# Kernel optimization log

Measured on AMD Instinct MI355X. Metric: run time of the kernel, lower is better.

Reference implementation:

```python
import jax, jax.numpy as jnp
import numpy as np

N_NODES = 50000
N_EDGES = 300000
F_IN, HID, N_CLS = 256, 256, 128


def _glorot_linear(key, fan_in, fan_out):
    # torch.nn.Linear-style uniform init, kaiming bound 1/sqrt(fan_in)
    s = 1.0 / np.sqrt(fan_in)
    return jax.random.uniform(key, (fan_in, fan_out), jnp.float32, -s, s)


def setup_inputs() -> dict:
    key = jax.random.key(0)
    ks = jax.random.split(key, 8)
    x = jax.random.normal(ks[0], (N_NODES, F_IN), jnp.float32)
    edge_index = jax.random.randint(ks[1], (2, N_EDGES), 0, N_NODES, dtype=jnp.int32)
    return {
        "x": x,
        "edge_index": edge_index,
        "W1": _glorot_linear(ks[2], F_IN, HID), "b1": jnp.zeros((HID,), jnp.float32),
        "W2": _glorot_linear(ks[3], HID, HID),  "b2": jnp.zeros((HID,), jnp.float32),
        "W3": _glorot_linear(ks[4], HID, HID),  "b3": jnp.zeros((HID,), jnp.float32),
        "W4": _glorot_linear(ks[5], HID, N_CLS), "b4": jnp.zeros((N_CLS,), jnp.float32),
    }


def _gcn_conv(x, W, b, src, dst, norm, n):
    # x' = D^{-1/2} (A + I) D^{-1/2} X W + b   (PyG GCNConv default)
    h = x @ W                                  # [N, out]
    msg = h[src] * norm[:, None]               # gather + edge scaling  [E', out]
    return jax.ops.segment_sum(msg, dst, num_segments=n) + b


def reference(x, edge_index, W1, b1, W2, b2, W3, b3, W4, b4):
    n = x.shape[0]
    loops = jnp.arange(n, dtype=edge_index.dtype)
    src = jnp.concatenate([edge_index[0], loops])  # add self-loops
    dst = jnp.concatenate([edge_index[1], loops])
    # symmetric normalization: deg over target nodes (unit edge weights)
    deg = jax.ops.segment_sum(jnp.ones_like(dst, jnp.float32), dst, num_segments=n)
    dis = jnp.where(deg > 0, jax.lax.rsqrt(jnp.maximum(deg, 1.0)), 0.0)
    norm = dis[src] * dis[dst]                     # [E']

    h = jax.nn.relu(_gcn_conv(x, W1, b1, src, dst, norm, n))
    h = jax.nn.relu(_gcn_conv(h, W2, b2, src, dst, norm, n))
    h = jax.nn.relu(_gcn_conv(h, W3, b3, src, dst, norm, n))
    h = _gcn_conv(h, W4, b4, src, dst, norm, n)    # [N, C]

    # global_add_pool with batch == zeros -> single-graph sum pool
    pooled = jnp.sum(h, axis=0, keepdims=True)     # [1, C]
    return (pooled, jax.nn.log_softmax(pooled, axis=1))
```

## Files before the change

### kernel.cpp

```cpp
#include <hip/hip_runtime.h>


typedef __attribute__((ext_vector_type(8))) short short8;
typedef __attribute__((ext_vector_type(4))) short short4v;
typedef __attribute__((ext_vector_type(4))) float float4v;

__device__ __forceinline__ unsigned short f2b(float f) {
    unsigned int u = __builtin_bit_cast(unsigned int, f);
    u += 0x7fffu + ((u >> 16) & 1u);
    return (unsigned short)(u >> 16);
}
__device__ __forceinline__ float b2f(unsigned short b) {
    unsigned int u = ((unsigned int)b) << 16;
    return __builtin_bit_cast(float, u);
}


__global__ void zero_kernel(int* __restrict__ cnt, float* __restrict__ tsum,
                            float* __restrict__ acc, int N) {
    int i = blockIdx.x * 256 + threadIdx.x;
    if (i < N) { cnt[i] = 0; tsum[i] = 0.f; }
    if (i < 256) acc[i] = 0.f;
}

__global__ void count_kernel(const int* __restrict__ dst, int* __restrict__ cnt, int E) {
    int i = blockIdx.x * blockDim.x + threadIdx.x;
    if (i < E) atomicAdd(&cnt[dst[i]], 1);
}

__global__ void blocksum_kernel(const int* __restrict__ cnt, int* __restrict__ bsum, int N) {
    __shared__ int s[256];
    int t = threadIdx.x;
    int i = blockIdx.x * 256 + t;
    s[t] = (i < N) ? cnt[i] : 0;
    __syncthreads();
    for (int d = 128; d > 0; d >>= 1) {
        if (t < d) s[t] += s[t + d];
        __syncthreads();
    }
    if (t == 0) bsum[blockIdx.x] = s[0];
}

__global__ void bscan_kernel(int* __restrict__ bsum, int B) {
    __shared__ int s[256];
    int t = threadIdx.x;
    int v = (t < B) ? bsum[t] : 0;
    s[t] = v;
    __syncthreads();
    for (int d = 1; d < 256; d <<= 1) {
        int x = (t >= d) ? s[t - d] : 0;
        __syncthreads();
        s[t] += x;
        __syncthreads();
    }
    if (t < B) bsum[t] = s[t] - v;
}

__global__ void finalize_kernel(const int* __restrict__ cnt, const int* __restrict__ bsum,
                                int* __restrict__ offs, int* __restrict__ cursor,
                                float* __restrict__ dis, int N, int E) {
    __shared__ int s[256];
    int t = threadIdx.x;
    int i = blockIdx.x * 256 + t;
    int c = (i < N) ? cnt[i] : 0;
    s[t] = c;
    __syncthreads();
    for (int d = 1; d < 256; d <<= 1) {
        int x = (t >= d) ? s[t - d] : 0;
        __syncthreads();
        s[t] += x;
        __syncthreads();
    }
    if (i < N) {
        int ex = bsum[blockIdx.x] + s[t] - c;
        offs[i] = ex;
        cursor[i] = ex;
        dis[i] = rsqrtf((float)(c + 1));
    }
    if (blockIdx.x == 0 && t == 0) offs[N] = E;
}

__global__ void scatter_outsum_kernel(const int* __restrict__ src, const int* __restrict__ dst,
                                      const float* __restrict__ dis, int* __restrict__ cursor,
                                      int* __restrict__ csr_src, float* __restrict__ csr_nrm,
                                      float* __restrict__ tsum, int E) {
    int i = blockIdx.x * blockDim.x + threadIdx.x;
    if (i < E) {
        int s = src[i], d = dst[i];
        float dd = dis[d];
        int pos = atomicAdd(&cursor[d], 1);
        csr_src[pos] = s;
        csr_nrm[pos] = dis[s] * dd;
        atomicAdd(&tsum[s], dd);
    }
}


__global__ void convert_wt_kernel(const float* __restrict__ W1, const float* __restrict__ W2,
                                  const float* __restrict__ W3, unsigned short* __restrict__ Wt1,
                                  unsigned short* __restrict__ Wt2, unsigned short* __restrict__ Wt3) {
    const float* W = (blockIdx.y == 0) ? W1 : (blockIdx.y == 1) ? W2 : W3;
    unsigned short* Wt = (blockIdx.y == 0) ? Wt1 : (blockIdx.y == 1) ? Wt2 : Wt3;
    int n = blockIdx.x;
    int k = threadIdx.x;
    Wt[n * 256 + k] = f2b(W[k * 256 + n]);
}

template <int AFP32>
__global__ __launch_bounds__(256, 3) void gemm_bf16_kernel(
        const void* __restrict__ Ap, const unsigned short* __restrict__ Wt,
        unsigned short* __restrict__ C, int M) {
    __shared__ unsigned short As[128 * 72];
    __shared__ unsigned short Bs[128 * 72];
    const int tid = threadIdx.x;
    const int lane = tid & 63;
    const int wave = tid >> 6;
    const int l15 = lane & 15;
    const int quad = lane >> 4;
    const int wm = wave & 1;
    const int wn = wave >> 1;
    const int m0 = blockIdx.x * 128;
    const int n0 = blockIdx.y * 128;

    float4v acc[4][4] = {};

    const int srow = tid >> 3;
    const int skof = (tid & 7) * 8;

    for (int kk = 0; kk < 256; kk += 64) {
#pragma unroll
        for (int p = 0; p < 4; p++) {
            int row = p * 32 + srow;
            int gm = m0 + row;
            if (AFP32) {
                const float* Af = (const float*)Ap;
                float4 lo = make_float4(0.f, 0.f, 0.f, 0.f);
                float4 hi = make_float4(0.f, 0.f, 0.f, 0.f);
                if (gm < M) {
                    lo = *(const float4*)&Af[(size_t)gm * 256 + kk + skof];
                    hi = *(const float4*)&Af[(size_t)gm * 256 + kk + skof + 4];
                }
                union { unsigned short u[8]; float4 v; } pk;
                pk.u[0] = f2b(lo.x); pk.u[1] = f2b(lo.y);
                pk.u[2] = f2b(lo.z); pk.u[3] = f2b(lo.w);
                pk.u[4] = f2b(hi.x); pk.u[5] = f2b(hi.y);
                pk.u[6] = f2b(hi.z); pk.u[7] = f2b(hi.w);
                *(float4*)&As[row * 72 + skof] = pk.v;
            } else {
                const unsigned short* Ab = (const unsigned short*)Ap;
                float4 av = make_float4(0.f, 0.f, 0.f, 0.f);
                if (gm < M) av = *(const float4*)&Ab[(size_t)gm * 256 + kk + skof];
                *(float4*)&As[row * 72 + skof] = av;
            }
            float4 bv = *(const float4*)&Wt[(size_t)(n0 + row) * 256 + kk + skof];
            *(float4*)&Bs[row * 72 + skof] = bv;
        }
        __syncthreads();
#pragma unroll
        for (int ks = 0; ks < 64; ks += 32) {
            short8 af[4], bf[4];
#pragma unroll
            for (int mi = 0; mi < 4; mi++)
                af[mi] = *(const short8*)&As[(wm * 64 + mi * 16 + l15) * 72 + ks + quad * 8];
#pragma unroll
            for (int nj = 0; nj < 4; nj++)
                bf[nj] = *(const short8*)&Bs[(wn * 64 + nj * 16 + l15) * 72 + ks + quad * 8];
#pragma unroll
            for (int mi = 0; mi < 4; mi++)
#pragma unroll
                for (int nj = 0; nj < 4; nj++)
                    acc[mi][nj] = __builtin_amdgcn_mfma_f32_16x16x32_bf16(
                        af[mi], bf[nj], acc[mi][nj], 0, 0, 0);
        }
        __syncthreads();
    }

#pragma unroll
    for (int mi = 0; mi < 4; mi++) {
#pragma unroll
        for (int r = 0; r < 4; r++) {
            int row = m0 + wm * 64 + mi * 16 + quad * 4 + r;
            if (row < M) {
#pragma unroll
                for (int nj = 0; nj < 4; nj++) {
                    int col = n0 + wn * 64 + nj * 16 + l15;
                    C[(size_t)row * 256 + col] = f2b(acc[mi][nj][r]);
                }
            }
        }
    }
}

template <int RELU>
__global__ __launch_bounds__(256) void agg_bf16_kernel(
        const unsigned short* __restrict__ T, const float* __restrict__ bias,
        const int* __restrict__ offs, const int* __restrict__ csr_src,
        const float* __restrict__ csr_nrm, const float* __restrict__ dis,
        unsigned short* __restrict__ out, int N) {
    int v = blockIdx.x * 8 + (threadIdx.x >> 5);
    if (v >= N) return;
    int l = threadIdx.x & 31;
    int f8 = l * 8;
    int beg = offs[v], end = offs[v + 1];
    float dv = dis[v];
    float w = dv * dv;
    float a[8];
    {
        short8 hs = *(const short8*)&T[(size_t)v * 256 + f8];
#pragma unroll
        for (int i = 0; i < 8; i++) a[i] = w * b2f((unsigned short)hs[i]);
    }
    int e = beg;
    for (; e + 4 <= end; e += 4) {
        int s0 = csr_src[e],     s1 = csr_src[e + 1];
        int s2 = csr_src[e + 2], s3 = csr_src[e + 3];
        float n0 = csr_nrm[e],     n1 = csr_nrm[e + 1];
        float n2 = csr_nrm[e + 2], n3 = csr_nrm[e + 3];
        short8 h0 = *(const short8*)&T[(size_t)s0 * 256 + f8];
        short8 h1 = *(const short8*)&T[(size_t)s1 * 256 + f8];
        short8 h2 = *(const short8*)&T[(size_t)s2 * 256 + f8];
        short8 h3 = *(const short8*)&T[(size_t)s3 * 256 + f8];
#pragma unroll
        for (int i = 0; i < 8; i++)
            a[i] += n0 * b2f((unsigned short)h0[i]) + n1 * b2f((unsigned short)h1[i])
                  + n2 * b2f((unsigned short)h2[i]) + n3 * b2f((unsigned short)h3[i]);
    }
    for (; e < end; e++) {
        int s = csr_src[e];
        float nm = csr_nrm[e];
        short8 h = *(const short8*)&T[(size_t)s * 256 + f8];
#pragma unroll
        for (int i = 0; i < 8; i++) a[i] += nm * b2f((unsigned short)h[i]);
    }
    float4 bv0 = *(const float4*)&bias[f8];
    float4 bv1 = *(const float4*)&bias[f8 + 4];
    a[0] += bv0.x; a[1] += bv0.y; a[2] += bv0.z; a[3] += bv0.w;
    a[4] += bv1.x; a[5] += bv1.y; a[6] += bv1.z; a[7] += bv1.w;
    if (RELU) {
#pragma unroll
        for (int i = 0; i < 8; i++) a[i] = fmaxf(a[i], 0.f);
    }
    uint4 o;
    o.x = (unsigned int)f2b(a[0]) | ((unsigned int)f2b(a[1]) << 16);
    o.y = (unsigned int)f2b(a[2]) | ((unsigned int)f2b(a[3]) << 16);
    o.z = (unsigned int)f2b(a[4]) | ((unsigned int)f2b(a[5]) << 16);
    o.w = (unsigned int)f2b(a[6]) | ((unsigned int)f2b(a[7]) << 16);
    *(uint4*)&out[(size_t)v * 256 + f8] = o;
}

__global__ __launch_bounds__(256) void wpool_partial(
        const unsigned short* __restrict__ H, const float* __restrict__ dis,
        const float* __restrict__ tsum, float* __restrict__ partial, int N) {
    int tid = threadIdx.x;
    int f8 = (tid & 31) * 8;
    int rg = tid >> 5;
    float a[8] = {};
    for (int r = blockIdx.x * 8 + rg; r < N; r += gridDim.x * 8) {
        float s = dis[r] * (dis[r] + tsum[r]);
        short8 h = *(const short8*)&H[(size_t)r * 256 + f8];
#pragma unroll
        for (int i = 0; i < 8; i++) a[i] += s * b2f((unsigned short)h[i]);
    }
    __shared__ float red[8 * 256];
#pragma unroll
    for (int i = 0; i < 8; i++) red[rg * 256 + f8 + i] = a[i];
    __syncthreads();
    for (int s = 4; s > 0; s >>= 1) {
        if (rg < s) {
#pragma unroll
            for (int i = 0; i < 8; i++)
                red[rg * 256 + f8 + i] += red[(rg + s) * 256 + f8 + i];
        }
        __syncthreads();
    }
    partial[(size_t)blockIdx.x * 256 + tid] = red[tid];
}

__global__ void wpool_reduce(const float* __restrict__ partial, float* __restrict__ acc) {
    int f = threadIdx.x;
    int p0 = blockIdx.x * 32;
    float a = 0.f;
#pragma unroll
    for (int p = 0; p < 32; p++) a += partial[(size_t)(p0 + p) * 256 + f];
    atomicAdd(&acc[f], a);
}

__global__ void final_kernel(const float* __restrict__ acc, const float* __restrict__ W4,
                             const float* __restrict__ b4, float* __restrict__ out, int N) {
    __shared__ float red[128];
    int c = threadIdx.x;
    float p = (float)N * b4[c];
    for (int k = 0; k < 256; k++) p += acc[k] * W4[k * 128 + c];
    out[c] = p;
    red[c] = p;
    __syncthreads();
    for (int s = 64; s > 0; s >>= 1) {
        if (c < s) red[c] = fmaxf(red[c], red[c + s]);
        __syncthreads();
    }
    float m = red[0];
    __syncthreads();
    red[c] = expf(p - m);
    __syncthreads();
    for (int s = 64; s > 0; s >>= 1) {
        if (c < s) red[c] += red[c + s];
        __syncthreads();
    }
    float lse = m + logf(red[0]);
    out[128 + c] = p - lse;
}

extern "C" void kernel_launch(void* const* d_in, const int* in_sizes, int n_in,
                              void* d_out, int out_size, void* d_ws, size_t ws_size,
                              hipStream_t stream) {
    const float* x  = (const float*)d_in[0];
    const int*   ei = (const int*)d_in[1];
    const float* W1 = (const float*)d_in[2];
    const float* b1 = (const float*)d_in[3];
    const float* W2 = (const float*)d_in[4];
    const float* b2 = (const float*)d_in[5];
    const float* W3 = (const float*)d_in[6];
    const float* b3 = (const float*)d_in[7];
    const float* W4 = (const float*)d_in[8];
    const float* b4 = (const float*)d_in[9];

    const int N = in_sizes[0] / 256;
    const int E = in_sizes[1] / 2;
    const int* src = ei;
    const int* dst = ei + E;

    char* p = (char*)d_ws;
    auto alloc = [&](size_t bytes) {
        char* r = p;
        p += (bytes + 255) & ~(size_t)255;
        return r;
    };
    int*            cnt     = (int*)alloc((size_t)N * 4);
    int*            offs    = (int*)alloc((size_t)(N + 1) * 4);
    int*            cursor  = (int*)alloc((size_t)N * 4);
    float*          dis     = (float*)alloc((size_t)N * 4);
    float*          tsum    = (float*)alloc((size_t)N * 4);
    int*            bsum    = (int*)alloc(1024 * 4);
    int*            csr_src = (int*)alloc((size_t)E * 4);
    float*          csr_nrm = (float*)alloc((size_t)E * 4);
    unsigned short* Wt1     = (unsigned short*)alloc(256 * 256 * 2);
    unsigned short* Wt2     = (unsigned short*)alloc(256 * 256 * 2);
    unsigned short* Wt3     = (unsigned short*)alloc(256 * 256 * 2);
    unsigned short* T       = (unsigned short*)alloc((size_t)N * 256 * 2);
    unsigned short* Abuf    = (unsigned short*)alloc((size_t)N * 256 * 2);
    float*          partial = (float*)alloc((size_t)1024 * 256 * 4);
    float*          accbuf  = (float*)alloc(256 * 4);

    int eb = (E + 255) / 256;
    int nb = (N + 255) / 256;
    zero_kernel<<<nb, 256, 0, stream>>>(cnt, tsum, accbuf, N);
    count_kernel<<<eb, 256, 0, stream>>>(dst, cnt, E);
    blocksum_kernel<<<nb, 256, 0, stream>>>(cnt, bsum, N);
    bscan_kernel<<<1, 256, 0, stream>>>(bsum, nb);
    finalize_kernel<<<nb, 256, 0, stream>>>(cnt, bsum, offs, cursor, dis, N, E);
    scatter_outsum_kernel<<<eb, 256, 0, stream>>>(src, dst, dis, cursor, csr_src,
                                                  csr_nrm, tsum, E);

    convert_wt_kernel<<<dim3(256, 3), 256, 0, stream>>>(W1, W2, W3, Wt1, Wt2, Wt3);

    dim3 ggrid((N + 127) / 128, 2);
    int ab = (N + 7) / 8;
    gemm_bf16_kernel<1><<<ggrid, 256, 0, stream>>>(x, Wt1, T, N);
    agg_bf16_kernel<1><<<ab, 256, 0, stream>>>(T, b1, offs, csr_src, csr_nrm, dis, Abuf, N);
    gemm_bf16_kernel<0><<<ggrid, 256, 0, stream>>>(Abuf, Wt2, T, N);
    agg_bf16_kernel<1><<<ab, 256, 0, stream>>>(T, b2, offs, csr_src, csr_nrm, dis, Abuf, N);
    gemm_bf16_kernel<0><<<ggrid, 256, 0, stream>>>(Abuf, Wt3, T, N);
    agg_bf16_kernel<1><<<ab, 256, 0, stream>>>(T, b3, offs, csr_src, csr_nrm, dis, Abuf, N);

    wpool_partial<<<1024, 256, 0, stream>>>(Abuf, dis, tsum, partial, N);
    wpool_reduce<<<32, 256, 0, stream>>>(partial, accbuf);
    final_kernel<<<1, 128, 0, stream>>>(accbuf, W4, b4, (float*)d_out, N);
}
```

Measured before the change: 334.2 us.

## Widen GEMM tile to full N with LDS-staged stores; fuse pooling into last aggregation

The GEMM now runs 512-thread blocks, each covering all 256 output columns for 128 rows, so every A tile is loaded once instead of twice. Results go through shared memory so global writes are coalesced 16-byte rows. The last aggregation kernel now also computes the weighted pooling partials per block, which removes the separate full pass that re-read the hidden activations. The cost is a 64KB LDS footprint that may limit occupancy, and a much larger partial buffer (one row per block) that the reduce kernel must scan.

```diff
diff --git a/kernel.cpp b/kernel.cpp
--- a/kernel.cpp
+++ b/kernel.cpp
@@ -2,7 +2,6 @@
 
 
 typedef __attribute__((ext_vector_type(8))) short short8;
-typedef __attribute__((ext_vector_type(4))) short short4v;
 typedef __attribute__((ext_vector_type(4))) float float4v;
 
 __device__ __forceinline__ unsigned short f2b(float f) {
@@ -107,11 +106,12 @@
 }
 
 template <int AFP32>
-__global__ __launch_bounds__(256, 3) void gemm_bf16_kernel(
+__global__ __launch_bounds__(512, 4) void gemm_bf16_kernel(
         const void* __restrict__ Ap, const unsigned short* __restrict__ Wt,
         unsigned short* __restrict__ C, int M) {
-    __shared__ unsigned short As[128 * 72];
-    __shared__ unsigned short Bs[128 * 72];
+    __shared__ __align__(16) unsigned char smem[65536];
+    unsigned short* As = (unsigned short*)smem;
+    unsigned short* Bs = (unsigned short*)(smem + 128 * 72 * 2);
     const int tid = threadIdx.x;
     const int lane = tid & 63;
     const int wave = tid >> 6;
@@ -120,7 +120,6 @@
     const int wm = wave & 1;
     const int wn = wave >> 1;
     const int m0 = blockIdx.x * 128;
-    const int n0 = blockIdx.y * 128;
 
     float4v acc[4][4] = {};
 
@@ -129,8 +128,8 @@
 
     for (int kk = 0; kk < 256; kk += 64) {
 #pragma unroll
-        for (int p = 0; p < 4; p++) {
-            int row = p * 32 + srow;
+        for (int p = 0; p < 2; p++) {
+            int row = p * 64 + srow;
             int gm = m0 + row;
             if (AFP32) {
                 const float* Af = (const float*)Ap;
@@ -152,7 +151,11 @@
                 if (gm < M) av = *(const float4*)&Ab[(size_t)gm * 256 + kk + skof];
                 *(float4*)&As[row * 72 + skof] = av;
             }
-            float4 bv = *(const float4*)&Wt[(size_t)(n0 + row) * 256 + kk + skof];
+        }
+#pragma unroll
+        for (int p = 0; p < 4; p++) {
+            int row = p * 64 + srow;
+            float4 bv = *(const float4*)&Wt[(size_t)row * 256 + kk + skof];
             *(float4*)&Bs[row * 72 + skof] = bv;
         }
         __syncthreads();
@@ -175,113 +178,110 @@
         __syncthreads();
     }
 
-#pragma unroll
-    for (int mi = 0; mi < 4; mi++) {
+    unsigned short* Cs = (unsigned short*)smem;
+#pragma unroll
+    for (int mi = 0; mi < 4; mi++)
 #pragma unroll
         for (int r = 0; r < 4; r++) {
-            int row = m0 + wm * 64 + mi * 16 + quad * 4 + r;
-            if (row < M) {
-#pragma unroll
-                for (int nj = 0; nj < 4; nj++) {
-                    int col = n0 + wn * 64 + nj * 16 + l15;
-                    C[(size_t)row * 256 + col] = f2b(acc[mi][nj][r]);
-                }
-            }
-        }
-    }
-}
-
-template <int RELU>
+            int row = wm * 64 + mi * 16 + quad * 4 + r;
+#pragma unroll
+            for (int nj = 0; nj < 4; nj++)
+                Cs[row * 256 + wn * 64 + nj * 16 + l15] = f2b(acc[mi][nj][r]);
+        }
+    __syncthreads();
+#pragma unroll
+    for (int i = 0; i < 8; i++) {
+        int g = i * 512 + tid;
+        int row = g >> 5;
+        int c8 = (g & 31) * 8;
+        if (m0 + row < M)
+            *(float4*)&C[(size_t)(m0 + row) * 256 + c8] = *(const float4*)&Cs[row * 256 + c8];
+    }
+}
+
+template <int RELU, int POOL>
 __global__ __launch_bounds__(256) void agg_bf16_kernel(
         const unsigned short* __restrict__ T, const float* __restrict__ bias,
         const int* __restrict__ offs, const int* __restrict__ csr_src,
         const float* __restrict__ csr_nrm, const float* __restrict__ dis,
-        unsigned short* __restrict__ out, int N) {
-    int v = blockIdx.x * 8 + (threadIdx.x >> 5);
-    if (v >= N) return;
+        unsigned short* __restrict__ out, int N,
+        const float* __restrict__ tsum, float* __restrict__ partial) {
+    int hw = threadIdx.x >> 5;
     int l = threadIdx.x & 31;
+    int v = blockIdx.x * 8 + hw;
     int f8 = l * 8;
-    int beg = offs[v], end = offs[v + 1];
-    float dv = dis[v];
-    float w = dv * dv;
-    float a[8];
-    {
-        short8 hs = *(const short8*)&T[(size_t)v * 256 + f8];
-#pragma unroll
-        for (int i = 0; i < 8; i++) a[i] = w * b2f((unsigned short)hs[i]);
-    }
-    int e = beg;
-    for (; e + 4 <= end; e += 4) {
-        int s0 = csr_src[e],     s1 = csr_src[e + 1];
-        int s2 = csr_src[e + 2], s3 = csr_src[e + 3];
-        float n0 = csr_nrm[e],     n1 = csr_nrm[e + 1];
-        float n2 = csr_nrm[e + 2], n3 = csr_nrm[e + 3];
-        short8 h0 = *(const short8*)&T[(size_t)s0 * 256 + f8];
-        short8 h1 = *(const short8*)&T[(size_t)s1 * 256 + f8];
-        short8 h2 = *(const short8*)&T[(size_t)s2 * 256 + f8];
-        short8 h3 = *(const short8*)&T[(size_t)s3 * 256 + f8];
-#pragma unroll
-        for (int i = 0; i < 8; i++)
-            a[i] += n0 * b2f((unsigned short)h0[i]) + n1 * b2f((unsigned short)h1[i])
-                  + n2 * b2f((unsigned short)h2[i]) + n3 * b2f((unsigned short)h3[i]);
-    }
-    for (; e < end; e++) {
-        int s = csr_src[e];
-        float nm = csr_nrm[e];
-        short8 h = *(const short8*)&T[(size_t)s * 256 + f8];
-#pragma unroll
-        for (int i = 0; i < 8; i++) a[i] += nm * b2f((unsigned short)h[i]);
-    }
-    float4 bv0 = *(const float4*)&bias[f8];
-    float4 bv1 = *(const float4*)&bias[f8 + 4];
-    a[0] += bv0.x; a[1] += bv0.y; a[2] += bv0.z; a[3] += bv0.w;
-    a[4] += bv1.x; a[5] += bv1.y; a[6] += bv1.z; a[7] += bv1.w;
-    if (RELU) {
-#pragma unroll
-        for (int i = 0; i < 8; i++) a[i] = fmaxf(a[i], 0.f);
-    }
-    uint4 o;
-    o.x = (unsigned int)f2b(a[0]) | ((unsigned int)f2b(a[1]) << 16);
-    o.y = (unsigned int)f2b(a[2]) | ((unsigned int)f2b(a[3]) << 16);
-    o.z = (unsigned int)f2b(a[4]) | ((unsigned int)f2b(a[5]) << 16);
-    o.w = (unsigned int)f2b(a[6]) | ((unsigned int)f2b(a[7]) << 16);
-    *(uint4*)&out[(size_t)v * 256 + f8] = o;
-}
-
-__global__ __launch_bounds__(256) void wpool_partial(
-        const unsigned short* __restrict__ H, const float* __restrict__ dis,
-        const float* __restrict__ tsum, float* __restrict__ partial, int N) {
-    int tid = threadIdx.x;
-    int f8 = (tid & 31) * 8;
-    int rg = tid >> 5;
     float a[8] = {};
-    for (int r = blockIdx.x * 8 + rg; r < N; r += gridDim.x * 8) {
-        float s = dis[r] * (dis[r] + tsum[r]);
-        short8 h = *(const short8*)&H[(size_t)r * 256 + f8];
-#pragma unroll
-        for (int i = 0; i < 8; i++) a[i] += s * b2f((unsigned short)h[i]);
-    }
-    __shared__ float red[8 * 256];
-#pragma unroll
-    for (int i = 0; i < 8; i++) red[rg * 256 + f8 + i] = a[i];
-    __syncthreads();
-    for (int s = 4; s > 0; s >>= 1) {
-        if (rg < s) {
+    float wv = 0.f;
+    if (v < N) {
+        int beg = offs[v], end = offs[v + 1];
+        float dv = dis[v];
+        float w = dv * dv;
+        {
+            short8 hs = *(const short8*)&T[(size_t)v * 256 + f8];
+#pragma unroll
+            for (int i = 0; i < 8; i++) a[i] = w * b2f((unsigned short)hs[i]);
+        }
+        int e = beg;
+        for (; e + 4 <= end; e += 4) {
+            int s0 = csr_src[e],     s1 = csr_src[e + 1];
+            int s2 = csr_src[e + 2], s3 = csr_src[e + 3];
+            float n0 = csr_nrm[e],     n1 = csr_nrm[e + 1];
+            float n2 = csr_nrm[e + 2], n3 = csr_nrm[e + 3];
+            short8 h0 = *(const short8*)&T[(size_t)s0 * 256 + f8];
+            short8 h1 = *(const short8*)&T[(size_t)s1 * 256 + f8];
+            short8 h2 = *(const short8*)&T[(size_t)s2 * 256 + f8];
+            short8 h3 = *(const short8*)&T[(size_t)s3 * 256 + f8];
 #pragma unroll
             for (int i = 0; i < 8; i++)
-                red[rg * 256 + f8 + i] += red[(rg + s) * 256 + f8 + i];
-        }
-        __syncthreads();
-    }
-    partial[(size_t)blockIdx.x * 256 + tid] = red[tid];
-}
-
-__global__ void wpool_reduce(const float* __restrict__ partial, float* __restrict__ acc) {
+                a[i] += n0 * b2f((unsigned short)h0[i]) + n1 * b2f((unsigned short)h1[i])
+                      + n2 * b2f((unsigned short)h2[i]) + n3 * b2f((unsigned short)h3[i]);
+        }
+        for (; e < end; e++) {
+            int s = csr_src[e];
+            float nm = csr_nrm[e];
+            short8 h = *(const short8*)&T[(size_t)s * 256 + f8];
+#pragma unroll
+            for (int i = 0; i < 8; i++) a[i] += nm * b2f((unsigned short)h[i]);
+        }
+        float4 bv0 = *(const float4*)&bias[f8];
+        float4 bv1 = *(const float4*)&bias[f8 + 4];
+        a[0] += bv0.x; a[1] += bv0.y; a[2] += bv0.z; a[3] += bv0.w;
+        a[4] += bv1.x; a[5] += bv1.y; a[6] += bv1.z; a[7] += bv1.w;
+        if (RELU) {
+#pragma unroll
+            for (int i = 0; i < 8; i++) a[i] = fmaxf(a[i], 0.f);
+        }
+        uint4 o;
+        o.x = (unsigned int)f2b(a[0]) | ((unsigned int)f2b(a[1]) << 16);
+        o.y = (unsigned int)f2b(a[2]) | ((unsigned int)f2b(a[3]) << 16);
+        o.z = (unsigned int)f2b(a[4]) | ((unsigned int)f2b(a[5]) << 16);
+        o.w = (unsigned int)f2b(a[6]) | ((unsigned int)f2b(a[7]) << 16);
+        *(uint4*)&out[(size_t)v * 256 + f8] = o;
+        if (POOL) wv = dv * (dv + tsum[v]);
+    }
+    if (POOL) {
+        __shared__ float red[2048];
+#pragma unroll
+        for (int i = 0; i < 8; i++) red[i * 256 + hw * 32 + l] = wv * a[i];
+        __syncthreads();
+        for (int s = 4; s > 0; s >>= 1) {
+            if (hw < s) {
+#pragma unroll
+                for (int i = 0; i < 8; i++)
+                    red[i * 256 + hw * 32 + l] += red[i * 256 + (hw + s) * 32 + l];
+            }
+            __syncthreads();
+        }
+        int f = threadIdx.x;
+        partial[(size_t)blockIdx.x * 256 + f] = red[(f & 7) * 256 + (f >> 3)];
+    }
+}
+
+__global__ void wpool_reduce(const float* __restrict__ partial, float* __restrict__ acc, int P) {
     int f = threadIdx.x;
-    int p0 = blockIdx.x * 32;
     float a = 0.f;
-#pragma unroll
-    for (int p = 0; p < 32; p++) a += partial[(size_t)(p0 + p) * 256 + f];
+    for (int p = blockIdx.x; p < P; p += gridDim.x)
+        a += partial[(size_t)p * 256 + f];
     atomicAdd(&acc[f], a);
 }
 
@@ -335,6 +335,8 @@
         p += (bytes + 255) & ~(size_t)255;
         return r;
     };
+    int ab = (N + 7) / 8;
+
     int*            cnt     = (int*)alloc((size_t)N * 4);
     int*            offs    = (int*)alloc((size_t)(N + 1) * 4);
     int*            cursor  = (int*)alloc((size_t)N * 4);
@@ -348,7 +350,7 @@
     unsigned short* Wt3     = (unsigned short*)alloc(256 * 256 * 2);
     unsigned short* T       = (unsigned short*)alloc((size_t)N * 256 * 2);
     unsigned short* Abuf    = (unsigned short*)alloc((size_t)N * 256 * 2);
-    float*          partial = (float*)alloc((size_t)1024 * 256 * 4);
+    float*          partial = (float*)alloc((size_t)ab * 256 * 4);
     float*          accbuf  = (float*)alloc(256 * 4);
 
     int eb = (E + 255) / 256;
@@ -363,16 +365,17 @@
 
     convert_wt_kernel<<<dim3(256, 3), 256, 0, stream>>>(W1, W2, W3, Wt1, Wt2, Wt3);
 
-    dim3 ggrid((N + 127) / 128, 2);
-    int ab = (N + 7) / 8;
-    gemm_bf16_kernel<1><<<ggrid, 256, 0, stream>>>(x, Wt1, T, N);
-    agg_bf16_kernel<1><<<ab, 256, 0, stream>>>(T, b1, offs, csr_src, csr_nrm, dis, Abuf, N);
-    gemm_bf16_kernel<0><<<ggrid, 256, 0, stream>>>(Abuf, Wt2, T, N);
-    agg_bf16_kernel<1><<<ab, 256, 0, stream>>>(T, b2, offs, csr_src, csr_nrm, dis, Abuf, N);
-    gemm_bf16_kernel<0><<<ggrid, 256, 0, stream>>>(Abuf, Wt3, T, N);
-    agg_bf16_kernel<1><<<ab, 256, 0, stream>>>(T, b3, offs, csr_src, csr_nrm, dis, Abuf, N);
-
-    wpool_partial<<<1024, 256, 0, stream>>>(Abuf, dis, tsum, partial, N);
-    wpool_reduce<<<32, 256, 0, stream>>>(partial, accbuf);
+    int ggrid = (N + 127) / 128;
+    gemm_bf16_kernel<1><<<ggrid, 512, 0, stream>>>(x, Wt1, T, N);
+    agg_bf16_kernel<1, 0><<<ab, 256, 0, stream>>>(T, b1, offs, csr_src, csr_nrm, dis,
+                                                  Abuf, N, nullptr, nullptr);
+    gemm_bf16_kernel<0><<<ggrid, 512, 0, stream>>>(Abuf, Wt2, T, N);
+    agg_bf16_kernel<1, 0><<<ab, 256, 0, stream>>>(T, b2, offs, csr_src, csr_nrm, dis,
+                                                  Abuf, N, nullptr, nullptr);
+    gemm_bf16_kernel<0><<<ggrid, 512, 0, stream>>>(Abuf, Wt3, T, N);
+    agg_bf16_kernel<1, 1><<<ab, 256, 0, stream>>>(T, b3, offs, csr_src, csr_nrm, dis,
+                                                  Abuf, N, tsum, partial);
+
+    wpool_reduce<<<64, 256, 0, stream>>>(partial, accbuf, ab);
     final_kernel<<<1, 128, 0, stream>>>(accbuf, W4, b4, (float*)d_out, N);
 }
```

After: 351.2 us. 1.05x slower.
